# Performance work log

Measured on AMD Instinct MI355X. Metric: run time of the kernel, lower is better.

Reference implementation:

```python
import jax, jax.numpy as jnp
import numpy as np

N, E, F, H, C, K = 50000, 1600000, 256, 6, 16, 40
NEG_SLOPE = 0.2  # PyG GATConv default
EPS = 1e-16


def _gat_layer(x, src, dst, W, a_s, a_d, b, heads, out_ch, concat):
    # linear transform per head: [N, heads, out_ch]
    h = (x @ W).reshape(N, heads, out_ch)
    # per-node attention logits
    al_s = jnp.einsum('nhc,hc->nh', h, a_s)  # source term
    al_d = jnp.einsum('nhc,hc->nh', h, a_d)  # destination term
    # edge-wise score + segment softmax over incoming edges of each dst node
    e = jax.nn.leaky_relu(al_s[src] + al_d[dst], NEG_SLOPE)  # [E', heads]
    m = jax.ops.segment_max(e, dst, num_segments=N)
    ex = jnp.exp(e - m[dst])
    denom = jax.ops.segment_sum(ex, dst, num_segments=N)
    alpha = ex / (denom[dst] + EPS)  # [E', heads]
    # weighted scatter-add aggregation
    out = jax.ops.segment_sum(h[src] * alpha[:, :, None], dst, num_segments=N)
    out = out.reshape(N, heads * out_ch) if concat else out.mean(axis=1)
    return out + b


def setup_inputs() -> dict:
    key = jax.random.key(0)
    ks = jax.random.split(key, 16)
    s = 0.05
    inp = {
        'x': jax.random.normal(ks[0], (N, F), dtype=jnp.float32),
        'edge_index': jax.random.randint(ks[1], (2, E), 0, N, dtype=jnp.int64 if jax.config.jax_enable_x64 else jnp.int32),
        'W1': jax.random.normal(ks[2], (F, H * C), dtype=jnp.float32) * s,
        'a1_s': jax.random.normal(ks[3], (H, C), dtype=jnp.float32) * s,
        'a1_d': jax.random.normal(ks[4], (H, C), dtype=jnp.float32) * s,
        'b1': jnp.zeros((H * C,), dtype=jnp.float32),
        'W2': jax.random.normal(ks[5], (H * C, H * C), dtype=jnp.float32) * s,
        'a2_s': jax.random.normal(ks[6], (H, C), dtype=jnp.float32) * s,
        'a2_d': jax.random.normal(ks[7], (H, C), dtype=jnp.float32) * s,
        'b2': jnp.zeros((H * C,), dtype=jnp.float32),
        'W3': jax.random.normal(ks[8], (H * C, H * C), dtype=jnp.float32) * s,
        'a3_s': jax.random.normal(ks[9], (H, C), dtype=jnp.float32) * s,
        'a3_d': jax.random.normal(ks[10], (H, C), dtype=jnp.float32) * s,
        'b3': jnp.zeros((H * C,), dtype=jnp.float32),
        'W4': jax.random.normal(ks[11], (H * C, K), dtype=jnp.float32) * s,
        'a4_s': jax.random.normal(ks[12], (1, K), dtype=jnp.float32) * s,
        'a4_d': jax.random.normal(ks[13], (1, K), dtype=jnp.float32) * s,
        'b4': jnp.zeros((K,), dtype=jnp.float32),
    }
    return inp


def reference(x, edge_index, W1, a1_s, a1_d, b1, W2, a2_s, a2_d, b2,
              W3, a3_s, a3_d, b3, W4, a4_s, a4_d, b4):
    # PyG GATConv adds self-loops by default
    loops = jnp.arange(N, dtype=edge_index.dtype)
    src = jnp.concatenate([edge_index[0], loops])
    dst = jnp.concatenate([edge_index[1], loops])
    # dropout is identity at eval time
    h = jax.nn.relu(_gat_layer(x, src, dst, W1, a1_s, a1_d, b1, H, C, True))
    h = jax.nn.relu(_gat_layer(h, src, dst, W2, a2_s, a2_d, b2, H, C, True))
    h = jax.nn.relu(_gat_layer(h, src, dst, W3, a3_s, a3_d, b3, H, C, True))
    h = _gat_layer(h, src, dst, W4, a4_s, a4_d, b4, 1, K, False)
    return jax.nn.log_softmax(h, axis=1)
```

## Files before the change

kernel.cpp:

```cpp
#include <hip/hip_runtime.h>
#include <cstdint>
#include <cstddef>

namespace {

constexpr int N  = 50000;
constexpr int E  = 1600000;
constexpr int ET = E + N;
constexpr int F  = 256;
constexpr int H  = 6;
constexpr int C  = 16;
constexpr int HC = H * C;
constexpr int K  = 40;
constexpr int SCAN_B = (N + 255) / 256;

typedef __attribute__((ext_vector_type(8))) short short8;
typedef __attribute__((ext_vector_type(4))) float f32x4;
typedef __attribute__((ext_vector_type(2))) float f32x2;

__device__ inline uint32_t f2bf(float f) {
  uint32_t u = __float_as_uint(f);
  return (u + 0x7FFFu + ((u >> 16) & 1u)) >> 16;
}
__device__ inline float bflo(uint32_t u) { return __uint_as_float(u << 16); }
__device__ inline float bfhi(uint32_t u) { return __uint_as_float(u & 0xFFFF0000u); }


__global__ void pos_kernel(const int* __restrict__ ei, int* __restrict__ deg8,
                           int* __restrict__ pos) {
  int e = blockIdx.x * 256 + threadIdx.x;
  if (e >= ET) return;
  int dst = (e < E) ? ei[E + e] : (e - E);
  int part = blockIdx.x & 7;
  pos[e] = atomicAdd(&deg8[part * N + dst], 1);
}

__global__ void combine_kernel(int* __restrict__ deg8, int* __restrict__ deg) {
  int i = blockIdx.x * 256 + threadIdx.x;
  if (i >= N) return;
  int s = 0;
#pragma unroll
  for (int p = 0; p < 8; p++) {
    int t = deg8[p * N + i];
    deg8[p * N + i] = s;
    s += t;
  }
  deg[i] = s;
}

__global__ void scan1_kernel(const int* __restrict__ deg, int* __restrict__ rowp,
                             int* __restrict__ bs) {
  __shared__ int s[256];
  int t = threadIdx.x;
  int i = blockIdx.x * 256 + t;
  int v = (i < N) ? deg[i] : 0;
  s[t] = v;
  __syncthreads();
  for (int off = 1; off < 256; off <<= 1) {
    int tv = (t >= off) ? s[t - off] : 0;
    __syncthreads();
    s[t] += tv;
    __syncthreads();
  }
  if (i < N) rowp[i] = s[t] - v;
  if (t == 255) bs[blockIdx.x] = s[255];
}

__global__ void scan2_kernel(int* __restrict__ bs, int* __restrict__ rowp) {
  __shared__ int s[256];
  int t = threadIdx.x;
  int v = (t < SCAN_B) ? bs[t] : 0;
  s[t] = v;
  __syncthreads();
  for (int off = 1; off < 256; off <<= 1) {
    int tv = (t >= off) ? s[t - off] : 0;
    __syncthreads();
    s[t] += tv;
    __syncthreads();
  }
  if (t < SCAN_B) bs[t] = s[t] - v;
  if (t == 255) rowp[N] = s[255];
}

__global__ void scan3_kernel(int* __restrict__ rowp, const int* __restrict__ bs) {
  int i = blockIdx.x * 256 + threadIdx.x;
  if (i < N) rowp[i] += bs[blockIdx.x];
}

__global__ void fill_kernel(const int* __restrict__ ei, const int* __restrict__ rowp,
                            const int* __restrict__ pos, const int* __restrict__ deg8,
                            int* __restrict__ col) {
  int e = blockIdx.x * 256 + threadIdx.x;
  if (e >= ET) return;
  int src, dst;
  if (e < E) { src = ei[e]; dst = ei[E + e]; }
  else       { src = e - E; dst = e - E; }
  int part = (e >> 8) & 7;
  col[rowp[dst] + deg8[part * N + dst] + pos[e]] = src;
}


__global__ void tobf16_kernel(const float* __restrict__ src, uint32_t* __restrict__ dst,
                              int n2) {
  int i = blockIdx.x * blockDim.x + threadIdx.x;
  if (i >= n2) return;
  float2 v = reinterpret_cast<const float2*>(src)[i];
  dst[i] = (f2bf(v.y) << 16) | f2bf(v.x);
}


__global__ void cvtW_kernel(const float* __restrict__ W1, const float* __restrict__ W2,
                            const float* __restrict__ W3, const float* __restrict__ W4,
                            uint16_t* __restrict__ WT1, uint16_t* __restrict__ WT2,
                            uint16_t* __restrict__ WT3, uint16_t* __restrict__ WT4) {
  constexpr int T1 = 96 * 256, T2 = 96 * 96, T3 = 96 * 96, T4 = 48 * 96;
  int t = blockIdx.x * blockDim.x + threadIdx.x;
  if (t < T1) {
    int n = t / 256, k = t % 256;
    WT1[t] = (uint16_t)f2bf(W1[(size_t)k * 96 + n]);
  } else if (t < T1 + T2) {
    int u = t - T1; int n = u / 96, k = u % 96;
    WT2[u] = (uint16_t)f2bf(W2[(size_t)k * 96 + n]);
  } else if (t < T1 + T2 + T3) {
    int u = t - T1 - T2; int n = u / 96, k = u % 96;
    WT3[u] = (uint16_t)f2bf(W3[(size_t)k * 96 + n]);
  } else if (t < T1 + T2 + T3 + T4) {
    int u = t - T1 - T2 - T3; int n = u / 96, k = u % 96;
    WT4[u] = (n < K) ? (uint16_t)f2bf(W4[(size_t)k * K + n]) : (uint16_t)0;
  }
}


template <int KD, int NT, int NCOLS, int OST>
__launch_bounds__(256)
__global__ void mfma_gemm_kernel(const uint32_t* __restrict__ A,
                                 const uint16_t* __restrict__ WT,
                                 uint16_t* __restrict__ hOut, int M) {
  constexpr int KU = KD / 2;
  const int wave = threadIdx.x >> 6;
  const int lane = threadIdx.x & 63;
  const int m0 = (blockIdx.x * 4 + wave) * 16;
  if (m0 >= M) return;
  const int r = lane & 15, g = lane >> 4;
  int rowA = m0 + r;
  if (rowA > M - 1) rowA = M - 1;
  const uint32_t* arow = A + (size_t)rowA * KU + g * 4;
  const uint32_t* wt32 = reinterpret_cast<const uint32_t*>(WT);

  f32x4 acc[NT];
#pragma unroll
  for (int nt = 0; nt < NT; nt++) acc[nt] = (f32x4){0.f, 0.f, 0.f, 0.f};

#pragma unroll
  for (int ks = 0; ks < KD / 32; ks++) {
    short8 av = *reinterpret_cast<const short8*>(arow + ks * 16);
#pragma unroll
    for (int nt = 0; nt < NT; nt++) {
      short8 bv = *reinterpret_cast<const short8*>(
          wt32 + (size_t)(nt * 16 + r) * KU + ks * 16 + g * 4);
      acc[nt] = __builtin_amdgcn_mfma_f32_16x16x32_bf16(av, bv, acc[nt], 0, 0, 0);
    }
  }

  const int orow = m0 + g * 4;
#pragma unroll
  for (int nt = 0; nt < NT; nt++) {
    const int ocol = nt * 16 + r;
#pragma unroll
    for (int t = 0; t < 4; t++) {
      int rr = orow + t;
      if (rr < M && ocol < NCOLS)
        hOut[(size_t)rr * OST + ocol] = (uint16_t)f2bf(acc[nt][t]);
    }
  }
}


__global__ void pack_kernel(const uint32_t* __restrict__ hB,
                            const float* __restrict__ as_, const float* __restrict__ ad_,
                            uint32_t* __restrict__ recs, float* __restrict__ aldP) {
  int t = blockIdx.x * 256 + threadIdx.x;
  if (t >= N * H) return;
  int n = t / H, hh = t % H;
  const uint32_t* hp = hB + (size_t)n * 48 + hh * 8;
  float f[16];
  float ss = 0.f, dd = 0.f;
#pragma unroll
  for (int i = 0; i < 8; i++) {
    uint32_t u = hp[i];
    f[2 * i] = bflo(u);
    f[2 * i + 1] = bfhi(u);
  }
#pragma unroll
  for (int c = 0; c < 16; c++) {
    ss += f[c] * as_[hh * 16 + c];
    dd += f[c] * ad_[hh * 16 + c];
  }
  uint32_t* rp = recs + (size_t)n * 32;
#pragma unroll
  for (int q = 0; q < 4; q++) {
    uint32_t w = 0;
    w = (uint32_t)__builtin_amdgcn_cvt_pk_fp8_f32(f[4 * q + 0], f[4 * q + 1], (int)w, false);
    w = (uint32_t)__builtin_amdgcn_cvt_pk_fp8_f32(f[4 * q + 2], f[4 * q + 3], (int)w, true);
    rp[hh * 4 + q] = w;
  }
  rp[24 + hh] = __float_as_uint(ss);
  aldP[(size_t)n * 8 + hh] = dd;
}


__global__ void pack4_kernel(const uint32_t* __restrict__ h4B,
                             const float* __restrict__ as_, const float* __restrict__ ad_,
                             uint32_t* __restrict__ recs4, float* __restrict__ ald4) {
  int n = blockIdx.x * 256 + threadIdx.x;
  if (n >= N) return;
  const uint32_t* hp = h4B + (size_t)n * 32;
  float f[40];
  float ss = 0.f, dd = 0.f;
#pragma unroll
  for (int i = 0; i < 20; i++) {
    uint32_t u = hp[i];
    f[2 * i] = bflo(u);
    f[2 * i + 1] = bfhi(u);
  }
#pragma unroll
  for (int c = 0; c < 40; c++) {
    ss += f[c] * as_[c];
    dd += f[c] * ad_[c];
  }
  uint32_t* rp = recs4 + (size_t)n * 16;
#pragma unroll
  for (int q = 0; q < 10; q++) {
    uint32_t w = 0;
    w = (uint32_t)__builtin_amdgcn_cvt_pk_fp8_f32(f[4 * q + 0], f[4 * q + 1], (int)w, false);
    w = (uint32_t)__builtin_amdgcn_cvt_pk_fp8_f32(f[4 * q + 2], f[4 * q + 3], (int)w, true);
    rp[q] = w;
  }
  rp[10] = __float_as_uint(ss);
  ald4[n] = dd;
}


template <int LPN, int NPW, int REC32, int ALSW, int HDIV, int PAD, bool LSM>
__launch_bounds__(256)
__global__ void flash_agg3_kernel(const uint32_t* __restrict__ recs,
                                  const int* __restrict__ rowp,
                                  const int* __restrict__ col,
                                  const float* __restrict__ aldP,
                                  const float* __restrict__ bias,
                                  uint4* __restrict__ outB4,
                                  float* __restrict__ outF32) {
  const int lane = threadIdx.x & 63;
  const int wave = threadIdx.x >> 6;
  int g = lane / LPN;
  const int li = lane - g * LPN;
  if (g > NPW - 1) g = NPW - 1;
  int n = (blockIdx.x * 4 + wave) * NPW + g;
  if (n > N - 1) n = N - 1;
  const int hh = li / HDIV;
  const float aldv = aldP[(size_t)n * PAD + hh];
  const int b0 = rowp[n];
  const int deg = rowp[n + 1] - b0;

  int km = deg;
#pragma unroll
  for (int off = 32; off > 0; off >>= 1) {
    int o = __shfl_xor(km, off);
    km = (o > km) ? o : km;
  }

  float a0 = 0.f, a1 = 0.f, a2 = 0.f, a3 = 0.f;
  float a4 = 0.f, a5 = 0.f, a6 = 0.f, a7 = 0.f;
  float ss = 0.f;

#pragma unroll 2
  for (int k = 0; k < km; k++) {
    bool valid = (k < deg);
    int j = b0 + (valid ? k : 0);
    int src = col[j];
    const uint32_t* rec = recs + (size_t)src * REC32;
    uint2 u = *reinterpret_cast<const uint2*>(rec + 2 * li);
    float l = __uint_as_float(rec[ALSW + hh]);
    float e = l + aldv;
    e = fmaxf(e, 0.2f * e);
    float p = __expf(e);
    p = valid ? p : 0.f;
    f32x2 c0 = __builtin_amdgcn_cvt_pk_f32_fp8((int)u.x, false);
    f32x2 c1 = __builtin_amdgcn_cvt_pk_f32_fp8((int)u.x, true);
    f32x2 c2 = __builtin_amdgcn_cvt_pk_f32_fp8((int)u.y, false);
    f32x2 c3 = __builtin_amdgcn_cvt_pk_f32_fp8((int)u.y, true);
    a0 += p * c0.x; a1 += p * c0.y;
    a2 += p * c1.x; a3 += p * c1.y;
    a4 += p * c2.x; a5 += p * c2.y;
    a6 += p * c3.x; a7 += p * c3.y;
    ss += p;
  }

  float inv = 1.f / (ss + 1e-16f);

  if (!LSM) {
    float o0 = fmaxf(a0 * inv + bias[8 * li + 0], 0.f);
    float o1 = fmaxf(a1 * inv + bias[8 * li + 1], 0.f);
    float o2 = fmaxf(a2 * inv + bias[8 * li + 2], 0.f);
    float o3 = fmaxf(a3 * inv + bias[8 * li + 3], 0.f);
    float o4 = fmaxf(a4 * inv + bias[8 * li + 4], 0.f);
    float o5 = fmaxf(a5 * inv + bias[8 * li + 5], 0.f);
    float o6 = fmaxf(a6 * inv + bias[8 * li + 6], 0.f);
    float o7 = fmaxf(a7 * inv + bias[8 * li + 7], 0.f);
    uint4 w;
    w.x = (f2bf(o1) << 16) | f2bf(o0);
    w.y = (f2bf(o3) << 16) | f2bf(o2);
    w.z = (f2bf(o5) << 16) | f2bf(o4);
    w.w = (f2bf(o7) << 16) | f2bf(o6);
    outB4[(size_t)n * LPN + li] = w;
  } else {
    bool vl = (li < 5);
    float v0 = vl ? a0 * inv + bias[8 * li + 0] : -1e30f;
    float v1 = vl ? a1 * inv + bias[8 * li + 1] : -1e30f;
    float v2 = vl ? a2 * inv + bias[8 * li + 2] : -1e30f;
    float v3 = vl ? a3 * inv + bias[8 * li + 3] : -1e30f;
    float v4 = vl ? a4 * inv + bias[8 * li + 4] : -1e30f;
    float v5 = vl ? a5 * inv + bias[8 * li + 5] : -1e30f;
    float v6 = vl ? a6 * inv + bias[8 * li + 6] : -1e30f;
    float v7 = vl ? a7 * inv + bias[8 * li + 7] : -1e30f;
    float mx = fmaxf(fmaxf(fmaxf(v0, v1), fmaxf(v2, v3)),
                     fmaxf(fmaxf(v4, v5), fmaxf(v6, v7)));
#pragma unroll
    for (int off = 1; off < 8; off <<= 1) mx = fmaxf(mx, __shfl_xor(mx, off));
    float es = 0.f;
    if (vl)
      es = __expf(v0 - mx) + __expf(v1 - mx) + __expf(v2 - mx) + __expf(v3 - mx) +
           __expf(v4 - mx) + __expf(v5 - mx) + __expf(v6 - mx) + __expf(v7 - mx);
#pragma unroll
    for (int off = 1; off < 8; off <<= 1) es += __shfl_xor(es, off);
    float lse = mx + __logf(es);
    if (vl) {
      float* op = outF32 + (size_t)n * K + li * 8;
      float4 w0 = make_float4(v0 - lse, v1 - lse, v2 - lse, v3 - lse);
      float4 w1 = make_float4(v4 - lse, v5 - lse, v6 - lse, v7 - lse);
      *reinterpret_cast<float4*>(op) = w0;
      *reinterpret_cast<float4*>(op + 4) = w1;
    }
  }
}

inline int cdiv(int a, int b) { return (a + b - 1) / b; }

}

extern "C" void kernel_launch(void* const* d_in, const int* in_sizes, int n_in,
                              void* d_out, int out_size, void* d_ws, size_t ws_size,
                              hipStream_t stream) {
  (void)in_sizes; (void)n_in; (void)out_size; (void)ws_size;
  const float* x   = (const float*)d_in[0];
  const int*   ei  = (const int*)d_in[1];
  const float* W1  = (const float*)d_in[2];
  const float* a1s = (const float*)d_in[3];
  const float* a1d = (const float*)d_in[4];
  const float* b1  = (const float*)d_in[5];
  const float* W2  = (const float*)d_in[6];
  const float* a2s = (const float*)d_in[7];
  const float* a2d = (const float*)d_in[8];
  const float* b2  = (const float*)d_in[9];
  const float* W3  = (const float*)d_in[10];
  const float* a3s = (const float*)d_in[11];
  const float* a3d = (const float*)d_in[12];
  const float* b3  = (const float*)d_in[13];
  const float* W4  = (const float*)d_in[14];
  const float* a4s = (const float*)d_in[15];
  const float* a4d = (const float*)d_in[16];
  const float* b4  = (const float*)d_in[17];
  float* out = (float*)d_out;

  char* ws = (char*)d_ws;
  size_t off = 0;
  auto alloc = [&](size_t bytes) {
    void* p = ws + off;
    off = (off + bytes + 255) & ~(size_t)255;
    return p;
  };
  int*      deg8  = (int*)alloc((size_t)8 * N * 4);
  int*      deg   = (int*)alloc((size_t)N * 4);
  int*      rowp  = (int*)alloc((size_t)(N + 1) * 4);
  int*      bs    = (int*)alloc((size_t)SCAN_B * 4);
  int*      pos   = (int*)alloc((size_t)ET * 4);
  int*      col   = (int*)alloc((size_t)ET * 4);
  uint32_t* xB    = (uint32_t*)alloc((size_t)N * (F / 2) * 4);
  uint16_t* WT1   = (uint16_t*)alloc((size_t)96 * 256 * 2);
  uint16_t* WT2   = (uint16_t*)alloc((size_t)96 * 96 * 2);
  uint16_t* WT3   = (uint16_t*)alloc((size_t)96 * 96 * 2);
  uint16_t* WT4   = (uint16_t*)alloc((size_t)48 * 96 * 2);
  uint32_t* hB    = (uint32_t*)alloc((size_t)N * (HC / 2) * 4);
  uint32_t* actB  = (uint32_t*)alloc((size_t)N * (HC / 2) * 4);
  uint32_t* h4B   = (uint32_t*)alloc((size_t)N * 32 * 4);
  uint32_t* recs  = (uint32_t*)alloc((size_t)N * 32 * 4);
  uint32_t* recs4 = (uint32_t*)alloc((size_t)N * 16 * 4);
  float*    aldP  = (float*)alloc((size_t)N * 8 * 4);

  hipMemsetAsync(deg8, 0, (size_t)8 * N * 4, stream);
  pos_kernel<<<cdiv(ET, 256), 256, 0, stream>>>(ei, deg8, pos);
  combine_kernel<<<cdiv(N, 256), 256, 0, stream>>>(deg8, deg);
  scan1_kernel<<<SCAN_B, 256, 0, stream>>>(deg, rowp, bs);
  scan2_kernel<<<1, 256, 0, stream>>>(bs, rowp);
  scan3_kernel<<<SCAN_B, 256, 0, stream>>>(rowp, bs);
  fill_kernel<<<cdiv(ET, 256), 256, 0, stream>>>(ei, rowp, pos, deg8, col);

  tobf16_kernel<<<cdiv(N * (F / 2), 256), 256, 0, stream>>>(x, xB, N * (F / 2));
  cvtW_kernel<<<cdiv(96 * 256 + 96 * 96 * 2 + 48 * 96, 256), 256, 0, stream>>>(
      W1, W2, W3, W4, WT1, WT2, WT3, WT4);

  const int gNH  = cdiv(N * H, 256);
  const int gN1  = cdiv(N, 256);
  const int gG   = cdiv(N, 64);
  const int gA96 = cdiv(N, 20);
  const int gA40 = cdiv(N, 32);

  mfma_gemm_kernel<F, 6, HC, HC><<<gG, 256, 0, stream>>>(xB, WT1, (uint16_t*)hB, N);
  pack_kernel<<<gNH, 256, 0, stream>>>(hB, a1s, a1d, recs, aldP);
  flash_agg3_kernel<12, 5, 32, 24, 2, 8, false><<<gA96, 256, 0, stream>>>(
      recs, rowp, col, aldP, b1, (uint4*)actB, nullptr);

  mfma_gemm_kernel<HC, 6, HC, HC><<<gG, 256, 0, stream>>>(actB, WT2, (uint16_t*)hB, N);
  pack_kernel<<<gNH, 256, 0, stream>>>(hB, a2s, a2d, recs, aldP);
  flash_agg3_kernel<12, 5, 32, 24, 2, 8, false><<<gA96, 256, 0, stream>>>(
      recs, rowp, col, aldP, b2, (uint4*)actB, nullptr);

  mfma_gemm_kernel<HC, 6, HC, HC><<<gG, 256, 0, stream>>>(actB, WT3, (uint16_t*)hB, N);
  pack_kernel<<<gNH, 256, 0, stream>>>(hB, a3s, a3d, recs, aldP);
  flash_agg3_kernel<12, 5, 32, 24, 2, 8, false><<<gA96, 256, 0, stream>>>(
      recs, rowp, col, aldP, b3, (uint4*)actB, nullptr);

  mfma_gemm_kernel<HC, 3, K, 64><<<gG, 256, 0, stream>>>(actB, WT4, (uint16_t*)h4B, N);
  pack4_kernel<<<gN1, 256, 0, stream>>>(h4B, a4s, a4d, recs4, aldP);
  flash_agg3_kernel<8, 8, 16, 10, 16, 1, true><<<gA40, 256, 0, stream>>>(
      recs4, rowp, col, aldP, b4, nullptr, out);
}
```

Before: 347.6 us.

## Rebuild CSR construction with destination-sliced counting and atomic fill passes

Replaces the per-edge position array and 8-way partitioned degree counters with two passes, each launching 8 blocks per edge chunk. Every block handles only destinations in one eighth of the node range, presumably to keep the atomic targets localized per XCD/L2. The fill pass claims slots with atomics instead of reading a precomputed position. This drops the pos array traffic and the combine kernel, but every edge chunk is now read 8 times, and the column order within a row becomes nondeterministic.

Result: slower. 411.4 us (+18.4%).

```diff
diff --git a/kernel.cpp b/kernel.cpp
--- a/kernel.cpp
+++ b/kernel.cpp
@@ -13,6 +13,9 @@
 constexpr int HC = H * C;
 constexpr int K  = 40;
 constexpr int SCAN_B = (N + 255) / 256;
+constexpr int SLICE = (N + 7) / 8;
+constexpr int EPB   = 4096;
+constexpr int CHUNKS = (ET + EPB - 1) / EPB;
 
 typedef __attribute__((ext_vector_type(8))) short short8;
 typedef __attribute__((ext_vector_type(4))) float f32x4;
@@ -26,26 +29,50 @@
 __device__ inline float bfhi(uint32_t u) { return __uint_as_float(u & 0xFFFF0000u); }
 
 
-__global__ void pos_kernel(const int* __restrict__ ei, int* __restrict__ deg8,
-                           int* __restrict__ pos) {
-  int e = blockIdx.x * 256 + threadIdx.x;
-  if (e >= ET) return;
-  int dst = (e < E) ? ei[E + e] : (e - E);
-  int part = blockIdx.x & 7;
-  pos[e] = atomicAdd(&deg8[part * N + dst], 1);
-}
-
-__global__ void combine_kernel(int* __restrict__ deg8, int* __restrict__ deg) {
-  int i = blockIdx.x * 256 + threadIdx.x;
-  if (i >= N) return;
-  int s = 0;
-#pragma unroll
-  for (int p = 0; p < 8; p++) {
-    int t = deg8[p * N + i];
-    deg8[p * N + i] = s;
-    s += t;
-  }
-  deg[i] = s;
+template <bool COUNT>
+__global__ void csr_pass_kernel(const int* __restrict__ ei,
+                                const int* __restrict__ rowp,
+                                int* __restrict__ cnt, int* __restrict__ col) {
+  const int slice = blockIdx.x & 7;
+  const int lo = slice * SLICE;
+  const int hi = (lo + SLICE < N) ? (lo + SLICE) : N;
+  const int base = (blockIdx.x >> 3) * EPB;
+  const int end = (base + EPB < ET) ? (base + EPB) : ET;
+
+  for (int e0 = base + (int)threadIdx.x * 4; e0 < end; e0 += 256 * 4) {
+    int d[4], s[4];
+    if (e0 + 3 < E) {
+      int4 dv = *reinterpret_cast<const int4*>(ei + E + e0);
+      d[0] = dv.x; d[1] = dv.y; d[2] = dv.z; d[3] = dv.w;
+      if (!COUNT) {
+        int4 sv = *reinterpret_cast<const int4*>(ei + e0);
+        s[0] = sv.x; s[1] = sv.y; s[2] = sv.z; s[3] = sv.w;
+      }
+    } else {
+#pragma unroll
+      for (int q = 0; q < 4; q++) {
+        int e = e0 + q;
+        if (e < ET) {
+          d[q] = (e < E) ? ei[E + e] : (e - E);
+          s[q] = (e < E) ? ei[e] : (e - E);
+        } else {
+          d[q] = -1; s[q] = -1;
+        }
+      }
+    }
+#pragma unroll
+    for (int q = 0; q < 4; q++) {
+      int dd = d[q];
+      if (dd >= lo && dd < hi) {
+        if (COUNT) {
+          atomicAdd(&cnt[dd], 1);
+        } else {
+          int p = atomicAdd(&cnt[dd], 1);
+          col[rowp[dd] + p] = s[q];
+        }
+      }
+    }
+  }
 }
 
 __global__ void scan1_kernel(const int* __restrict__ deg, int* __restrict__ rowp,
@@ -85,18 +112,6 @@
 __global__ void scan3_kernel(int* __restrict__ rowp, const int* __restrict__ bs) {
   int i = blockIdx.x * 256 + threadIdx.x;
   if (i < N) rowp[i] += bs[blockIdx.x];
-}
-
-__global__ void fill_kernel(const int* __restrict__ ei, const int* __restrict__ rowp,
-                            const int* __restrict__ pos, const int* __restrict__ deg8,
-                            int* __restrict__ col) {
-  int e = blockIdx.x * 256 + threadIdx.x;
-  if (e >= ET) return;
-  int src, dst;
-  if (e < E) { src = ei[e]; dst = ei[E + e]; }
-  else       { src = e - E; dst = e - E; }
-  int part = (e >> 8) & 7;
-  col[rowp[dst] + deg8[part * N + dst] + pos[e]] = src;
 }
 
 
@@ -379,11 +394,10 @@
     off = (off + bytes + 255) & ~(size_t)255;
     return p;
   };
-  int*      deg8  = (int*)alloc((size_t)8 * N * 4);
   int*      deg   = (int*)alloc((size_t)N * 4);
+  int*      fillc = (int*)alloc((size_t)N * 4);
   int*      rowp  = (int*)alloc((size_t)(N + 1) * 4);
   int*      bs    = (int*)alloc((size_t)SCAN_B * 4);
-  int*      pos   = (int*)alloc((size_t)ET * 4);
   int*      col   = (int*)alloc((size_t)ET * 4);
   uint32_t* xB    = (uint32_t*)alloc((size_t)N * (F / 2) * 4);
   uint16_t* WT1   = (uint16_t*)alloc((size_t)96 * 256 * 2);
@@ -397,13 +411,13 @@
   uint32_t* recs4 = (uint32_t*)alloc((size_t)N * 16 * 4);
   float*    aldP  = (float*)alloc((size_t)N * 8 * 4);
 
-  hipMemsetAsync(deg8, 0, (size_t)8 * N * 4, stream);
-  pos_kernel<<<cdiv(ET, 256), 256, 0, stream>>>(ei, deg8, pos);
-  combine_kernel<<<cdiv(N, 256), 256, 0, stream>>>(deg8, deg);
+  hipMemsetAsync(deg, 0, (size_t)N * 4, stream);
+  hipMemsetAsync(fillc, 0, (size_t)N * 4, stream);
+  csr_pass_kernel<true><<<CHUNKS * 8, 256, 0, stream>>>(ei, nullptr, deg, nullptr);
   scan1_kernel<<<SCAN_B, 256, 0, stream>>>(deg, rowp, bs);
   scan2_kernel<<<1, 256, 0, stream>>>(bs, rowp);
   scan3_kernel<<<SCAN_B, 256, 0, stream>>>(rowp, bs);
-  fill_kernel<<<cdiv(ET, 256), 256, 0, stream>>>(ei, rowp, pos, deg8, col);
+  csr_pass_kernel<false><<<CHUNKS * 8, 256, 0, stream>>>(ei, rowp, fillc, col);
 
   tobf16_kernel<<<cdiv(N * (F / 2), 256), 256, 0, stream>>>(x, xB, N * (F / 2));
   cvtW_kernel<<<cdiv(96 * 256 + 96 * 96 * 2 + 48 * 96, 256), 256, 0, stream>>>(
```
